# Kernel optimization log

Hardware: AMD Instinct MI355X
Metric: run time of the kernel (lower is better)

## Reference

```python
import jax, jax.numpy as jnp
import numpy as np

SEQ, MEM, B, H, NH, HD = 1024, 1024, 4, 1024, 16, 64
TOT = SEQ + MEM
RLEN = TOT
SCALE = 1.0 / np.sqrt(HD).astype(np.float32)
LN_EPS = 1e-5


def setup_inputs() -> dict:
    key = jax.random.key(0)
    ks = jax.random.split(key, 10)
    w = 0.02  # weight init scale
    # causal mask over memory+current segment: query i may attend keys j <= i + MEM
    i = jnp.arange(SEQ)[:, None]
    j = jnp.arange(TOT)[None, :]
    mask2d = j > (i + MEM)  # [SEQ, TOT] bool
    attn_mask = jnp.broadcast_to(mask2d[:, :, None], (SEQ, TOT, B))
    return {
        "x": jax.random.normal(ks[0], (SEQ, B, H), jnp.float32),
        "pos_embed": jax.random.normal(ks[1], (RLEN, H), jnp.float32),
        "r_w_bias": jax.random.normal(ks[2], (NH, HD), jnp.float32) * w,
        "r_r_bias": jax.random.normal(ks[3], (NH, HD), jnp.float32) * w,
        "attn_mask": attn_mask,
        "memory": jax.random.normal(ks[4], (MEM, B, H), jnp.float32),
        "W_qkv": jax.random.normal(ks[5], (3 * NH * HD, H), jnp.float32) * w,
        "W_r": jax.random.normal(ks[6], (NH * HD, H), jnp.float32) * w,
        "W_o": jax.random.normal(ks[7], (H, NH * HD), jnp.float32) * w,
        "ln_w": jnp.ones((H,), jnp.float32),
        "ln_b": jnp.zeros((H,), jnp.float32),
    }


def _layer_norm(x, w, b):
    mu = jnp.mean(x, axis=-1, keepdims=True)
    var = jnp.mean(jnp.square(x - mu), axis=-1, keepdims=True)
    return (x - mu) * jax.lax.rsqrt(var + LN_EPS) * w + b


def _rel_shift(x):
    # x: [i, j, b, n]; TXL rel-shift via pad-reshape-drop trick
    i, j, b, n = x.shape
    zp = jnp.zeros((i, 1, b, n), x.dtype)
    xp = jnp.concatenate([zp, x], axis=1)          # [i, j+1, b, n]
    xp = xp.reshape(j + 1, i, b, n)                # reinterpret row-major layout
    return xp[1:].reshape(i, j, b, n)


def reference(x, pos_embed, r_w_bias, r_r_bias, attn_mask, memory, W_qkv, W_r, W_o, ln_w, ln_b):
    full = jnp.concatenate([memory, x], axis=0)    # [TOT, B, H]
    w_heads = full @ W_qkv.T                       # [TOT, B, 3*NH*HD]
    q, k, v = jnp.split(w_heads, 3, axis=-1)
    q = q[-SEQ:].reshape(SEQ, B, NH, HD)
    k = k.reshape(TOT, B, NH, HD)
    v = v.reshape(TOT, B, NH, HD)
    r_k = (pos_embed @ W_r.T).reshape(RLEN, NH, HD)

    attn_ac = jnp.einsum('ibnd,jbnd->ijbn', q + r_w_bias, k)   # content score
    attn_bd = jnp.einsum('ibnd,jnd->ijbn', q + r_r_bias, r_k)  # position score
    attn_bd = _rel_shift(attn_bd)
    score = (attn_ac + attn_bd) * SCALE            # [SEQ, TOT, B, NH]
    score = jnp.where(attn_mask[:, :, :, None], -jnp.inf, score)
    prob = jax.nn.softmax(score, axis=1)           # softmax over key dim
    # dropout layers are identity in eval mode
    attn_vec = jnp.einsum('ijbn,jbnd->ibnd', prob, v).reshape(SEQ, B, NH * HD)
    attn_out = attn_vec @ W_o.T                    # [SEQ, B, H]
    return _layer_norm(x + attn_out, ln_w, ln_b)   # post-LN (pre_lnorm=False)
```

## Files before the change

kernel.cpp:

```cpp
#include <hip/hip_runtime.h>
#include <stdint.h>

typedef unsigned short u16;
typedef __bf16 bf16t;
typedef bf16t bf16x8 __attribute__((ext_vector_type(8)));
typedef float f32x4 __attribute__((ext_vector_type(4)));

#define DEV static __device__ __forceinline__

DEV u16 f2b(float f) {
  unsigned u = __float_as_uint(f);
  return (u16)((u + 0x7fffu + ((u >> 16) & 1u)) >> 16);
}
DEV u16 bcast(float f) {
  union { bf16t b; u16 u; } c;
  c.b = (bf16t)f;
  return c.u;
}
DEV float b2f(u16 h) { return __uint_as_float(((unsigned)h) << 16); }
DEV f32x4 fzero() { f32x4 v = {0.f, 0.f, 0.f, 0.f}; return v; }
DEV f32x4 mfma16(bf16x8 a, bf16x8 b, f32x4 c) {
  return __builtin_amdgcn_mfma_f32_16x16x32_bf16(a, b, c, 0, 0, 0);
}
DEV float exp2fast(float x) { return __builtin_amdgcn_exp2f(x); }
DEV void gload16(const u16* g, u16* l) {
  __builtin_amdgcn_global_load_lds(
      (const __attribute__((address_space(1))) unsigned int*)g,
      (__attribute__((address_space(3))) unsigned int*)l, 16, 0, 0);
}

#define SEQ 1024
#define MEML 1024
#define BB 4
#define HH 1024
#define NHH 16
#define HDD 64
#define TOT 2048


__global__ __launch_bounds__(256) void k_pack(const float* __restrict__ mem,
                                              const float* __restrict__ x,
                                              u16* __restrict__ full) {
  size_t id4 = (size_t)blockIdx.x * 256 + threadIdx.x;
  size_t base = id4 * 4;
  int t = (int)(base >> 12);
  int rem = (int)(base & 4095);
  const float* src = (t < MEML) ? (mem + ((size_t)t << 12) + rem)
                                : (x + ((size_t)(t - MEML) << 12) + rem);
  float4 v = *(const float4*)src;
  ushort4 o;
  o.x = f2b(v.x); o.y = f2b(v.y); o.z = f2b(v.z); o.w = f2b(v.w);
  *(ushort4*)(full + base) = o;
}

__global__ __launch_bounds__(256) void k_cvt(const float* __restrict__ src,
                                             u16* __restrict__ dst, int n4) {
  int id = blockIdx.x * 256 + threadIdx.x;
  if (id >= n4) return;
  size_t base = (size_t)id * 4;
  float4 v = *(const float4*)(src + base);
  ushort4 o;
  o.x = f2b(v.x); o.y = f2b(v.y); o.z = f2b(v.z); o.w = f2b(v.w);
  *(ushort4*)(dst + base) = o;
}


template <int MF, int NF>
DEV void gemm_core2(const u16* __restrict__ A, int lda,
                    const u16* __restrict__ Bt, int ldb, int K,
                    f32x4 (&acc)[MF][NF]) {
  __shared__ __align__(16) u16 As[128 * 32];
  __shared__ __align__(16) u16 Bs[128 * 32];
  const int tid = threadIdx.x, lane = tid & 63, wave = tid >> 6;
  const int l15 = lane & 15, g = lane >> 4;
  const int wm = wave >> 1, wn = wave & 1;
#pragma unroll
  for (int fm = 0; fm < MF; ++fm)
#pragma unroll
    for (int fn = 0; fn < NF; ++fn) acc[fm][fn] = fzero();

  const int e8a = tid, e8b = 256 + tid;
  const int ra0 = e8a >> 2, ca0 = (e8a & 3) << 3;
  const int ra1 = e8b >> 2, ca1 = (e8b & 3) << 3;
  u16* asd0 = As + (wave << 9);
  u16* asd1 = As + 2048 + (wave << 9);
  u16* bsd0 = Bs + (wave << 9);
  u16* bsd1 = Bs + 2048 + (wave << 9);

  for (int k0 = 0; k0 < K; k0 += 32) {
    __syncthreads();
    gload16(A + (size_t)ra0 * lda + k0 + ca0, asd0);
    gload16(A + (size_t)ra1 * lda + k0 + ca1, asd1);
    gload16(Bt + (size_t)ra0 * ldb + k0 + ca0, bsd0);
    gload16(Bt + (size_t)ra1 * ldb + k0 + ca1, bsd1);
    __syncthreads();
    bf16x8 af[MF], bfr[NF];
#pragma unroll
    for (int fm = 0; fm < MF; ++fm)
      af[fm] = *(const bf16x8*)(As + ((wm * 64 + fm * 16 + l15) << 5) + (g << 3));
#pragma unroll
    for (int fn = 0; fn < NF; ++fn)
      bfr[fn] = *(const bf16x8*)(Bs + ((wn * 64 + fn * 16 + l15) << 5) + (g << 3));
#pragma unroll
    for (int fm = 0; fm < MF; ++fm)
#pragma unroll
      for (int fn = 0; fn < NF; ++fn)
        acc[fm][fn] = mfma16(af[fm], bfr[fn], acc[fm][fn]);
  }
}

template <int BM, int BN, int MF, int NF, class F>
DEV void epi_apply(f32x4 (&acc)[MF][NF], F&& f) {
  constexpr int WAVES_N = BN / (16 * NF);
  const int lane = threadIdx.x & 63, wave = threadIdx.x >> 6;
  const int wm = wave / WAVES_N, wn = wave % WAVES_N;
#pragma unroll
  for (int fm = 0; fm < MF; ++fm)
#pragma unroll
    for (int fn = 0; fn < NF; ++fn)
#pragma unroll
      for (int q = 0; q < 4; ++q) {
        int rl = wm * (16 * MF) + fm * 16 + ((lane >> 4) << 2) + q;
        int cl = wn * (16 * NF) + fn * 16 + (lane & 15);
        f(rl, cl, acc[fm][fn][q]);
      }
}


__global__ __launch_bounds__(256) void k_gemm_qkv(
    const u16* __restrict__ full, const u16* __restrict__ wqkv,
    const float* __restrict__ rwb, const float* __restrict__ rrb,
    u16* __restrict__ qw, u16* __restrict__ qr, u16* __restrict__ kk,
    u16* __restrict__ vt) {
  f32x4 acc[4][4];
  const u16* A = full + (size_t)blockIdx.x * 128 * 1024;
  const u16* Bt = wqkv + (size_t)blockIdx.y * 128 * 1024;
  gemm_core2<4, 4>(A, 1024, Bt, 1024, 1024, acc);
  const int row0 = blockIdx.x * 128, col0 = blockIdx.y * 128;
  epi_apply<128, 128, 4, 4>(acc, [&](int rl, int cl, float v) {
    int grow = row0 + rl, gcol = col0 + cl;
    int t = grow >> 2, bb = grow & 3;
    int which = gcol >> 10, hd = gcol & 1023;
    int n = hd >> 6, d = hd & 63;
    if (which == 0) {
      if (t >= MEML) {
        int i = t - MEML;
        size_t o = ((size_t)(bb * NHH + n) * SEQ + i) * HDD + d;
        qw[o] = f2b(v + rwb[hd]);
        qr[o] = f2b(v + rrb[hd]);
      }
    } else if (which == 1) {
      kk[((size_t)(bb * NHH + n) * TOT + t) * HDD + d] = f2b(v);
    } else {
      vt[((size_t)(bb * NHH + n) * HDD + d) * TOT + t] = f2b(v);
    }
  });
}

__global__ __launch_bounds__(256) void k_gemm_rk(const u16* __restrict__ pos,
                                                 const u16* __restrict__ wr,
                                                 u16* __restrict__ rk) {
  f32x4 acc[4][4];
  const u16* A = pos + (size_t)blockIdx.x * 128 * 1024;
  const u16* Bt = wr + (size_t)blockIdx.y * 128 * 1024;
  gemm_core2<4, 4>(A, 1024, Bt, 1024, 1024, acc);
  const int row0 = blockIdx.x * 128, col0 = blockIdx.y * 128;
  epi_apply<128, 128, 4, 4>(acc, [&](int rl, int cl, float v) {
    int r = row0 + rl, o = col0 + cl;
    int n = o >> 6, d = o & 63;
    rk[((size_t)n * TOT + r) * HDD + d] = f2b(v);
  });
}

__global__ __launch_bounds__(256) void k_gemm_out(const u16* __restrict__ avec,
                                                  const u16* __restrict__ wo,
                                                  const float* __restrict__ x,
                                                  float* __restrict__ y) {
  f32x4 acc[4][4];
  const u16* A = avec + (size_t)blockIdx.x * 128 * 1024;
  const u16* Bt = wo + (size_t)blockIdx.y * 128 * 1024;
  gemm_core2<4, 4>(A, 1024, Bt, 1024, 1024, acc);
  const int row0 = blockIdx.x * 128, col0 = blockIdx.y * 128;
  epi_apply<128, 128, 4, 4>(acc, [&](int rl, int cl, float v) {
    size_t o = (size_t)(row0 + rl) * HH + (col0 + cl);
    y[o] = v + x[o];
  });
}


__global__ __launch_bounds__(256, 2) void k_flash(
    const u16* __restrict__ qw, const u16* __restrict__ qr,
    const u16* __restrict__ kk, const u16* __restrict__ rk,
    const u16* __restrict__ vt, u16* __restrict__ avec) {
  __shared__ __align__(16) u16 Kb[2 * 4096];
  __shared__ __align__(16) u16 Vb[2 * 4096];
  __shared__ __align__(16) u16 BDp[64 * 136];
  __shared__ __align__(16) u16 Ps[4 * 1024];
  const int tid = threadIdx.x, lane = tid & 63, w = tid >> 6;
  const int l15 = lane & 15, g = lane >> 4;
  const int bid = blockIdx.x;
  const int work = (bid & 7) * 128 + (bid >> 3);
  const int ti = 15 - (work & 15);
  const int pair = work >> 4;
  const int n = pair & 15, b = pair >> 4;
  const int i0 = ti * 64;
  const int bn = b * NHH + n;
  const u16* qwb = qw + ((size_t)bn * SEQ + i0) * HDD;
  const u16* qrb = qr + ((size_t)bn * SEQ + i0) * HDD;
  const u16* kbase = kk + (size_t)bn * TOT * HDD;
  const u16* rbase = rk + (size_t)n * TOT * HDD;
  const u16* vbase = vt + (size_t)bn * HDD * TOT;

  bf16x8 qwf[2], qrf[2];
#pragma unroll
  for (int ks = 0; ks < 2; ++ks) {
    int off = (w * 16 + l15) * HDD + ks * 32 + (g << 3);
    qwf[ks] = *(const bf16x8*)(qwb + off);
    qrf[ks] = *(const bf16x8*)(qrb + off);
  }

  const float NEGINF = -__builtin_inff();
  const float C2 = 0.125f * 1.44269504089f;
  f32x4 oacc[4];
#pragma unroll
  for (int db = 0; db < 4; ++db) oacc[db] = fzero();
  float mrow[4] = {NEGINF, NEGINF, NEGINF, NEGINF};
  float lrow[4] = {0.f, 0.f, 0.f, 0.f};

  const int m0 = 15 - ti;
  const int jtc = ti + 17;

  const int sr = (w << 4) + (lane >> 3);
  const int sc = (lane & 7) << 3;

  int bd_rd[16], bd_rs[16];
#pragma unroll
  for (int fn = 0; fn < 4; ++fn)
#pragma unroll
    for (int q = 0; q < 4; ++q) {
      int di = (w << 4) + (g << 2) + q;
      int dj = (fn << 4) + l15;
      int rl = (63 + dj - di) & 63;
      int s0 = ((1023 - i0 + dj - di) >> 6) & 1;
      int a0 = rl * 136 + s0 * 68 + di;
      int a1 = rl * 136 + (s0 ^ 1) * 68 + di;
      bd_rd[fn * 4 + q] = a0;
      bd_rs[fn * 4 + q] = a0 + a1;
    }
  int bd_wr[4], bd_ws[4];
  {
    int colw = (w << 4) + (g << 2);
    int sA = m0 & 1;
#pragma unroll
    for (int fn = 0; fn < 4; ++fn) {
      int wl = (fn << 4) + l15;
      int a0 = wl * 136 + sA * 68 + colw;
      int a1 = wl * 136 + (sA ^ 1) * 68 + colw;
      bd_wr[fn] = a0;
      bd_ws[fn] = a0 + a1;
    }
  }
  int ps_wr[16];
#pragma unroll
  for (int fn = 0; fn < 4; ++fn)
#pragma unroll
    for (int q = 0; q < 4; ++q) {
      int row = (g << 2) + q;
      ps_wr[fn * 4 + q] =
          (w << 10) + (row << 6) + ((((fn << 4) + l15)) ^ ((row & 7) << 3));
    }
  const int psr0 = (w << 10) + (l15 << 6) + ((g << 3) ^ ((l15 & 7) << 3));
  const int psr1 = psr0 ^ 32;
  int kr0 = (l15 << 6) + ((g << 3) ^ ((l15 & 7) << 3));
  int kr1 = kr0 ^ 32;
  int vr0 = kr0, vr1 = kr1;
  const int kwb = (sr << 6) + (sc ^ ((sr & 7) << 3));

  int koff = (64 + sr) * 64 + sc;
  int voff0 = sr * 2048 + 64 + sc;
  int voff1 = voff0 + 8 * 2048;
  int rvo[4];
#pragma unroll
  for (int fn = 0; fn < 4; ++fn)
    rvo[fn] = (((m0 + 2) << 6) + (fn << 4) + l15) * 64 + (g << 3);

  uint4 kg0, kg1, vg0, vg1;
  bf16x8 rfr[8];

  auto bd_comp_store = [&]() {
    f32x4 bd[4];
#pragma unroll
    for (int fn = 0; fn < 4; ++fn) bd[fn] = fzero();
#pragma unroll
    for (int ks = 0; ks < 2; ++ks)
#pragma unroll
      for (int fn = 0; fn < 4; ++fn)
        bd[fn] = mfma16(qrf[ks], rfr[ks * 4 + fn], bd[fn]);
#pragma unroll
    for (int fn = 0; fn < 4; ++fn) {
      ushort4 pk = {bcast(bd[fn][0] * C2), bcast(bd[fn][1] * C2),
                    bcast(bd[fn][2] * C2), bcast(bd[fn][3] * C2)};
      *(ushort4*)(BDp + bd_wr[fn]) = pk;
      bd_wr[fn] = bd_ws[fn] - bd_wr[fn];
    }
  };

  kg0 = *(const uint4*)(kbase + sr * 64 + sc);
  kg1 = *(const uint4*)(kbase + (sr + 8) * 64 + sc);
  vg0 = *(const uint4*)(vbase + sr * 2048 + sc);
  vg1 = *(const uint4*)(vbase + (sr + 8) * 2048 + sc);
#pragma unroll
  for (int fn = 0; fn < 4; ++fn) {
    int ro = ((m0 << 6) + (fn << 4) + l15) * 64 + (g << 3);
#pragma unroll
    for (int ks = 0; ks < 2; ++ks)
      rfr[ks * 4 + fn] = *(const bf16x8*)(rbase + ro + ks * 32);
  }
  bd_comp_store();
#pragma unroll
  for (int fn = 0; fn < 4; ++fn) {
    int ro = (((m0 + 1) << 6) + (fn << 4) + l15) * 64 + (g << 3);
#pragma unroll
    for (int ks = 0; ks < 2; ++ks)
      rfr[ks * 4 + fn] = *(const bf16x8*)(rbase + ro + ks * 32);
  }
  bd_comp_store();
  *(uint4*)(Kb + kwb) = kg0;
  *(uint4*)(Kb + kwb + 512) = kg1;
  *(uint4*)(Vb + kwb) = vg0;
  *(uint4*)(Vb + kwb + 512) = vg1;
  __syncthreads();
  int kw = kwb ^ 4096;

  for (int jt = 0; jt < jtc; ++jt) {
    const bool haveStage = (jt + 1 < jtc);
    const bool haveBD = (jt + 3 <= jtc);
    if (haveStage) {
      kg0 = *(const uint4*)(kbase + koff);
      kg1 = *(const uint4*)(kbase + koff + 512);
      vg0 = *(const uint4*)(vbase + voff0);
      vg1 = *(const uint4*)(vbase + voff1);
    }
    if (haveBD) {
#pragma unroll
      for (int fn = 0; fn < 4; ++fn)
#pragma unroll
        for (int ks = 0; ks < 2; ++ks)
          rfr[ks * 4 + fn] = *(const bf16x8*)(rbase + rvo[fn] + ks * 32);
    }

    f32x4 ac[4];
#pragma unroll
    for (int fn = 0; fn < 4; ++fn) ac[fn] = fzero();
#pragma unroll
    for (int fn = 0; fn < 4; ++fn) {
      bf16x8 kf = *(const bf16x8*)(Kb + kr0 + fn * 1024);
      ac[fn] = mfma16(qwf[0], kf, ac[fn]);
    }
#pragma unroll
    for (int fn = 0; fn < 4; ++fn) {
      bf16x8 kf = *(const bf16x8*)(Kb + kr1 + fn * 1024);
      ac[fn] = mfma16(qwf[1], kf, ac[fn]);
    }

    const bool last = (jt == jtc - 1);
    float pmax[4] = {NEGINF, NEGINF, NEGINF, NEGINF};
#pragma unroll
    for (int fn = 0; fn < 4; ++fn)
#pragma unroll
      for (int q = 0; q < 4; ++q) {
        float bdv = b2f(BDp[bd_rd[fn * 4 + q]]);
        float sv = __builtin_fmaf(ac[fn][q], C2, bdv);
        if (last) {
          int di = (g << 2) + q;
          int dj = (fn << 4) + l15 - (w << 4);
          if (dj > di) sv = NEGINF;
        }
        ac[fn][q] = sv;
        pmax[q] = fmaxf(pmax[q], sv);
      }
#pragma unroll
    for (int q = 0; q < 4; ++q) {
#pragma unroll
      for (int off = 1; off < 16; off <<= 1)
        pmax[q] = fmaxf(pmax[q], __shfl_xor(pmax[q], off, 64));
    }
    int need = (pmax[0] > mrow[0] + 8.f) | (pmax[1] > mrow[1] + 8.f) |
               (pmax[2] > mrow[2] + 8.f) | (pmax[3] > mrow[3] + 8.f);
    if (__any(need)) {
#pragma unroll
      for (int q = 0; q < 4; ++q) {
        float mn = fmaxf(mrow[q], pmax[q]);
        float sc2 = exp2fast(mrow[q] - mn);
        mrow[q] = mn;
        lrow[q] *= sc2;
#pragma unroll
        for (int db = 0; db < 4; ++db) oacc[db][q] *= sc2;
      }
    }
#pragma unroll
    for (int fn = 0; fn < 4; ++fn)
#pragma unroll
      for (int q = 0; q < 4; ++q) {
        float p = exp2fast(ac[fn][q] - mrow[q]);
        lrow[q] += p;
        Ps[ps_wr[fn * 4 + q]] = bcast(p);
      }
    {
      bf16x8 pa0 = *(const bf16x8*)(Ps + psr0);
      bf16x8 pa1 = *(const bf16x8*)(Ps + psr1);
#pragma unroll
      for (int db = 0; db < 4; ++db) {
        bf16x8 vf = *(const bf16x8*)(Vb + vr0 + db * 1024);
        oacc[db] = mfma16(pa0, vf, oacc[db]);
      }
#pragma unroll
      for (int db = 0; db < 4; ++db) {
        bf16x8 vf = *(const bf16x8*)(Vb + vr1 + db * 1024);
        oacc[db] = mfma16(pa1, vf, oacc[db]);
      }
    }
    if (haveBD) bd_comp_store();
    if (haveStage) {
      *(uint4*)(Kb + kw) = kg0;
      *(uint4*)(Kb + kw + 512) = kg1;
      *(uint4*)(Vb + kw) = vg0;
      *(uint4*)(Vb + kw + 512) = vg1;
    }
    __syncthreads();
#pragma unroll
    for (int e = 0; e < 16; ++e) bd_rd[e] = bd_rs[e] - bd_rd[e];
    kr0 ^= 4096; kr1 ^= 4096; vr0 ^= 4096; vr1 ^= 4096; kw ^= 4096;
    koff += 4096; voff0 += 64; voff1 += 64;
#pragma unroll
    for (int fn = 0; fn < 4; ++fn) rvo[fn] += 4096;
  }

#pragma unroll
  for (int q = 0; q < 4; ++q) {
#pragma unroll
    for (int off = 1; off < 16; off <<= 1)
      lrow[q] += __shfl_xor(lrow[q], off, 64);
    lrow[q] = 1.f / lrow[q];
  }
#pragma unroll
  for (int db = 0; db < 4; ++db)
#pragma unroll
    for (int q = 0; q < 4; ++q) {
      int i = i0 + (w << 4) + (g << 2) + q;
      avec[((size_t)i * BB + b) * HH + n * HDD + db * 16 + l15] =
          bcast(oacc[db][q] * lrow[q]);
    }
}


__global__ __launch_bounds__(256) void k_ln(const float* __restrict__ y,
                                            const float* __restrict__ lw,
                                            const float* __restrict__ lb,
                                            float* __restrict__ out) {
  const int row = blockIdx.x, tid = threadIdx.x;
  const float4 v = *(const float4*)(y + (size_t)row * HH + tid * 4);
  float s = v.x + v.y + v.z + v.w;
  float ss = v.x * v.x + v.y * v.y + v.z * v.z + v.w * v.w;
#pragma unroll
  for (int off = 1; off < 64; off <<= 1) {
    s += __shfl_xor(s, off, 64);
    ss += __shfl_xor(ss, off, 64);
  }
  __shared__ float red[8];
  const int w = tid >> 6, lane = tid & 63;
  if (lane == 0) { red[w] = s; red[4 + w] = ss; }
  __syncthreads();
  float tot = red[0] + red[1] + red[2] + red[3];
  float tss = red[4] + red[5] + red[6] + red[7];
  float mu = tot * (1.f / 1024.f);
  float var = tss * (1.f / 1024.f) - mu * mu;
  float rs = rsqrtf(var + 1e-5f);
  float4 wv = *(const float4*)(lw + tid * 4);
  float4 bv = *(const float4*)(lb + tid * 4);
  float4 o;
  o.x = (v.x - mu) * rs * wv.x + bv.x;
  o.y = (v.y - mu) * rs * wv.y + bv.y;
  o.z = (v.z - mu) * rs * wv.z + bv.z;
  o.w = (v.w - mu) * rs * wv.w + bv.w;
  *(float4*)(out + (size_t)row * HH + tid * 4) = o;
}


extern "C" void kernel_launch(void* const* d_in, const int* in_sizes, int n_in,
                              void* d_out, int out_size, void* d_ws,
                              size_t ws_size, hipStream_t stream) {
  const float* x = (const float*)d_in[0];
  const float* pos = (const float*)d_in[1];
  const float* rwb = (const float*)d_in[2];
  const float* rrb = (const float*)d_in[3];
  const float* mem = (const float*)d_in[5];
  const float* wqkv = (const float*)d_in[6];
  const float* wr = (const float*)d_in[7];
  const float* wo = (const float*)d_in[8];
  const float* lnw = (const float*)d_in[9];
  const float* lnb = (const float*)d_in[10];

  char* ws = (char*)d_ws;
  const size_t O_FULL = 0;
  const size_t O_WQKV = 16777216;
  const size_t O_WR = 23068672;
  const size_t O_WO = 25165824;
  const size_t O_POS = 27262976;
  const size_t O_QW = 31457280;
  const size_t O_QR = 39845888;
  const size_t O_K = 48234496;
  const size_t O_VT = 65011712;
  const size_t O_RK = 81788928;
  const size_t O_AVEC = 85983232;
  const size_t NEED = 94371840;

  if (ws_size < NEED) return;

  u16* full = (u16*)(ws + O_FULL);
  u16* wqkv_b = (u16*)(ws + O_WQKV);
  u16* wr_b = (u16*)(ws + O_WR);
  u16* wo_b = (u16*)(ws + O_WO);
  u16* pos_b = (u16*)(ws + O_POS);
  u16* qw = (u16*)(ws + O_QW);
  u16* qr = (u16*)(ws + O_QR);
  u16* kk = (u16*)(ws + O_K);
  u16* vt = (u16*)(ws + O_VT);
  u16* rk = (u16*)(ws + O_RK);
  u16* avec = (u16*)(ws + O_AVEC);
  float* y = (float*)(ws + O_FULL);

  k_pack<<<8192, 256, 0, stream>>>(mem, x, full);
  k_cvt<<<3072, 256, 0, stream>>>(wqkv, wqkv_b, 786432);
  k_cvt<<<1024, 256, 0, stream>>>(wr, wr_b, 262144);
  k_cvt<<<1024, 256, 0, stream>>>(wo, wo_b, 262144);
  k_cvt<<<2048, 256, 0, stream>>>(pos, pos_b, 524288);

  k_gemm_qkv<<<dim3(64, 24), 256, 0, stream>>>(full, wqkv_b, rwb, rrb, qw, qr,
                                               kk, vt);
  k_gemm_rk<<<dim3(16, 8), 256, 0, stream>>>(pos_b, wr_b, rk);

  k_flash<<<dim3(1024), 256, 0, stream>>>(qw, qr, kk, rk, vt, avec);

  k_gemm_out<<<dim3(32, 8), 256, 0, stream>>>(avec, wo_b, x, y);
  k_ln<<<4096, 256, 0, stream>>>(y, lnw, lnb, (float*)d_out);
}
```

Measured before the change: 300.5 us.

## Transpose flash-attention MFMA operands for per-lane rows; merge weight-conversion kernels

The flash kernel swaps the MFMA A/B operands so each lane holds a single query row with 16 key columns. This turns the per-row max and sum reductions from four 4-step shuffles into one scalar with two shuffles, and makes the P stores and output stores 4-wide vectors. The four separate fp32-to-bf16 weight conversion launches are merged into one kernel that writes a contiguous destination, which assumes the bf16 weight buffers sit back to back in the workspace. The BD read indexing and the causal mask are re-derived for the transposed layout, which risks indexing errors.

New measurement: 289.7 us. 1.04x faster.

```diff
diff --git a/kernel.cpp b/kernel.cpp
--- a/kernel.cpp
+++ b/kernel.cpp
@@ -53,12 +53,19 @@
   *(ushort4*)(full + base) = o;
 }
 
-__global__ __launch_bounds__(256) void k_cvt(const float* __restrict__ src,
-                                             u16* __restrict__ dst, int n4) {
-  int id = blockIdx.x * 256 + threadIdx.x;
-  if (id >= n4) return;
-  size_t base = (size_t)id * 4;
-  float4 v = *(const float4*)(src + base);
+__global__ __launch_bounds__(256) void k_cvt4(const float* __restrict__ s0,
+                                              const float* __restrict__ s1,
+                                              const float* __restrict__ s2,
+                                              const float* __restrict__ s3,
+                                              u16* __restrict__ dst) {
+  size_t base = ((size_t)blockIdx.x * 256 + threadIdx.x) * 4;
+  const float* src;
+  size_t off;
+  if (base < 3145728) { src = s0; off = base; }
+  else if (base < 4194304) { src = s1; off = base - 3145728; }
+  else if (base < 5242880) { src = s2; off = base - 4194304; }
+  else { src = s3; off = base - 5242880; }
+  float4 v = *(const float4*)(src + off);
   ushort4 o;
   o.x = f2b(v.x); o.y = f2b(v.y); o.z = f2b(v.z); o.w = f2b(v.w);
   *(ushort4*)(dst + base) = o;
@@ -224,8 +231,7 @@
   f32x4 oacc[4];
 #pragma unroll
   for (int db = 0; db < 4; ++db) oacc[db] = fzero();
-  float mrow[4] = {NEGINF, NEGINF, NEGINF, NEGINF};
-  float lrow[4] = {0.f, 0.f, 0.f, 0.f};
+  float mrow = NEGINF, lrow = 0.f;
 
   const int m0 = 15 - ti;
   const int jtc = ti + 17;
@@ -233,13 +239,13 @@
   const int sr = (w << 4) + (lane >> 3);
   const int sc = (lane & 7) << 3;
 
+  const int di = (w << 4) + l15;
   int bd_rd[16], bd_rs[16];
 #pragma unroll
   for (int fn = 0; fn < 4; ++fn)
 #pragma unroll
     for (int q = 0; q < 4; ++q) {
-      int di = (w << 4) + (g << 2) + q;
-      int dj = (fn << 4) + l15;
+      int dj = (fn << 4) + (g << 2) + q;
       int rl = (63 + dj - di) & 63;
       int s0 = ((1023 - i0 + dj - di) >> 6) & 1;
       int a0 = rl * 136 + s0 * 68 + di;
@@ -260,17 +266,14 @@
       bd_ws[fn] = a0 + a1;
     }
   }
-  int ps_wr[16];
+  const int psX = (l15 & 3) << 1;
+  int ps_w[4];
 #pragma unroll
   for (int fn = 0; fn < 4; ++fn)
-#pragma unroll
-    for (int q = 0; q < 4; ++q) {
-      int row = (g << 2) + q;
-      ps_wr[fn * 4 + q] =
-          (w << 10) + (row << 6) + ((((fn << 4) + l15)) ^ ((row & 7) << 3));
-    }
-  const int psr0 = (w << 10) + (l15 << 6) + ((g << 3) ^ ((l15 & 7) << 3));
-  const int psr1 = psr0 ^ 32;
+    ps_w[fn] = (w << 10) + (l15 << 6) + (((fn << 1) + (g >> 1)) ^ psX) * 8 +
+               ((g & 1) << 2);
+  const int psr0 = (w << 10) + (l15 << 6) + ((g ^ psX) * 8);
+  const int psr1 = (w << 10) + (l15 << 6) + (((4 + g) ^ psX) * 8);
   int kr0 = (l15 << 6) + ((g << 3) ^ ((l15 & 7) << 3));
   int kr1 = kr0 ^ 32;
   int vr0 = kr0, vr1 = kr1;
@@ -355,69 +358,60 @@
 #pragma unroll
     for (int fn = 0; fn < 4; ++fn) {
       bf16x8 kf = *(const bf16x8*)(Kb + kr0 + fn * 1024);
-      ac[fn] = mfma16(qwf[0], kf, ac[fn]);
+      ac[fn] = mfma16(kf, qwf[0], ac[fn]);
     }
 #pragma unroll
     for (int fn = 0; fn < 4; ++fn) {
       bf16x8 kf = *(const bf16x8*)(Kb + kr1 + fn * 1024);
-      ac[fn] = mfma16(qwf[1], kf, ac[fn]);
+      ac[fn] = mfma16(kf, qwf[1], ac[fn]);
     }
 
     const bool last = (jt == jtc - 1);
-    float pmax[4] = {NEGINF, NEGINF, NEGINF, NEGINF};
+    float pm = NEGINF;
 #pragma unroll
     for (int fn = 0; fn < 4; ++fn)
 #pragma unroll
       for (int q = 0; q < 4; ++q) {
         float bdv = b2f(BDp[bd_rd[fn * 4 + q]]);
         float sv = __builtin_fmaf(ac[fn][q], C2, bdv);
-        if (last) {
-          int di = (g << 2) + q;
-          int dj = (fn << 4) + l15 - (w << 4);
-          if (dj > di) sv = NEGINF;
-        }
+        if (last && ((fn << 4) + (g << 2) + q > di)) sv = NEGINF;
         ac[fn][q] = sv;
-        pmax[q] = fmaxf(pmax[q], sv);
+        pm = fmaxf(pm, sv);
       }
-#pragma unroll
-    for (int q = 0; q < 4; ++q) {
-#pragma unroll
-      for (int off = 1; off < 16; off <<= 1)
-        pmax[q] = fmaxf(pmax[q], __shfl_xor(pmax[q], off, 64));
-    }
-    int need = (pmax[0] > mrow[0] + 8.f) | (pmax[1] > mrow[1] + 8.f) |
-               (pmax[2] > mrow[2] + 8.f) | (pmax[3] > mrow[3] + 8.f);
-    if (__any(need)) {
-#pragma unroll
-      for (int q = 0; q < 4; ++q) {
-        float mn = fmaxf(mrow[q], pmax[q]);
-        float sc2 = exp2fast(mrow[q] - mn);
-        mrow[q] = mn;
-        lrow[q] *= sc2;
-#pragma unroll
-        for (int db = 0; db < 4; ++db) oacc[db][q] *= sc2;
-      }
-    }
-#pragma unroll
-    for (int fn = 0; fn < 4; ++fn)
-#pragma unroll
-      for (int q = 0; q < 4; ++q) {
-        float p = exp2fast(ac[fn][q] - mrow[q]);
-        lrow[q] += p;
-        Ps[ps_wr[fn * 4 + q]] = bcast(p);
-      }
+    pm = fmaxf(pm, __shfl_xor(pm, 16, 64));
+    pm = fmaxf(pm, __shfl_xor(pm, 32, 64));
+    if (__any(pm > mrow + 8.f)) {
+      float mn = fmaxf(mrow, pm);
+      float sc2 = exp2fast(mrow - mn);
+      mrow = mn;
+      lrow *= sc2;
+#pragma unroll
+      for (int db = 0; db < 4; ++db)
+#pragma unroll
+        for (int q = 0; q < 4; ++q) oacc[db][q] *= sc2;
+    }
+#pragma unroll
+    for (int fn = 0; fn < 4; ++fn) {
+      float p0 = exp2fast(ac[fn][0] - mrow);
+      float p1 = exp2fast(ac[fn][1] - mrow);
+      float p2 = exp2fast(ac[fn][2] - mrow);
+      float p3 = exp2fast(ac[fn][3] - mrow);
+      lrow += (p0 + p1) + (p2 + p3);
+      ushort4 pk = {bcast(p0), bcast(p1), bcast(p2), bcast(p3)};
+      *(ushort4*)(Ps + ps_w[fn]) = pk;
+    }
     {
       bf16x8 pa0 = *(const bf16x8*)(Ps + psr0);
       bf16x8 pa1 = *(const bf16x8*)(Ps + psr1);
 #pragma unroll
       for (int db = 0; db < 4; ++db) {
         bf16x8 vf = *(const bf16x8*)(Vb + vr0 + db * 1024);
-        oacc[db] = mfma16(pa0, vf, oacc[db]);
+        oacc[db] = mfma16(vf, pa0, oacc[db]);
       }
 #pragma unroll
       for (int db = 0; db < 4; ++db) {
         bf16x8 vf = *(const bf16x8*)(Vb + vr1 + db * 1024);
-        oacc[db] = mfma16(pa1, vf, oacc[db]);
+        oacc[db] = mfma16(vf, pa1, oacc[db]);
       }
     }
     if (haveBD) bd_comp_store();
@@ -436,21 +430,17 @@
     for (int fn = 0; fn < 4; ++fn) rvo[fn] += 4096;
   }
 
-#pragma unroll
-  for (int q = 0; q < 4; ++q) {
-#pragma unroll
-    for (int off = 1; off < 16; off <<= 1)
-      lrow[q] += __shfl_xor(lrow[q], off, 64);
-    lrow[q] = 1.f / lrow[q];
-  }
-#pragma unroll
-  for (int db = 0; db < 4; ++db)
-#pragma unroll
-    for (int q = 0; q < 4; ++q) {
-      int i = i0 + (w << 4) + (g << 2) + q;
-      avec[((size_t)i * BB + b) * HH + n * HDD + db * 16 + l15] =
-          bcast(oacc[db][q] * lrow[q]);
-    }
+  lrow += __shfl_xor(lrow, 16, 64);
+  lrow += __shfl_xor(lrow, 32, 64);
+  const float linv = 1.f / lrow;
+  const int arow = (i0 + (w << 4) + l15) * BB + b;
+  u16* abase = avec + (size_t)arow * HH + n * HDD + (g << 2);
+#pragma unroll
+  for (int db = 0; db < 4; ++db) {
+    ushort4 o = {bcast(oacc[db][0] * linv), bcast(oacc[db][1] * linv),
+                 bcast(oacc[db][2] * linv), bcast(oacc[db][3] * linv)};
+    *(ushort4*)(abase + db * 16) = o;
+  }
 }
 
 
@@ -531,10 +521,7 @@
   float* y = (float*)(ws + O_FULL);
 
   k_pack<<<8192, 256, 0, stream>>>(mem, x, full);
-  k_cvt<<<3072, 256, 0, stream>>>(wqkv, wqkv_b, 786432);
-  k_cvt<<<1024, 256, 0, stream>>>(wr, wr_b, 262144);
-  k_cvt<<<1024, 256, 0, stream>>>(wo, wo_b, 262144);
-  k_cvt<<<2048, 256, 0, stream>>>(pos, pos_b, 524288);
+  k_cvt4<<<7168, 256, 0, stream>>>(wqkv, wr, wo, pos, wqkv_b);
 
   k_gemm_qkv<<<dim3(64, 24), 256, 0, stream>>>(full, wqkv_b, rwb, rrb, qw, qr,
                                                kk, vt);
```
